# Performance work log

Hardware: AMD Instinct MI355X
Metric: run time of the kernel (lower is better)

The kernel has to match this reference:

```python
import jax, jax.numpy as jnp
import numpy as np

B, D, E, K = 8192, 4096, 64, 2

def setup_inputs() -> dict:
    key = jax.random.key(0)
    k1, k2 = jax.random.split(key)
    x = jax.random.normal(k1, (B, D), dtype=jnp.float32)
    gate_w = jax.random.normal(k2, (E, D), dtype=jnp.float32) * (1.0 / np.sqrt(D))
    temperature = jnp.ones((), dtype=jnp.float32)
    return {"x": x, "gate_w": gate_w, "temperature": temperature}

def reference(x, gate_w, temperature):
    # logits = (x @ W^T) / temperature  -> [B, E]
    logits = jnp.einsum('bd,ed->be', x, gate_w) / temperature
    top_logits, top_idx = jax.lax.top_k(logits, K)          # [B, K]
    routing_weights = jax.nn.softmax(top_logits, axis=-1)    # [B, K]
    rows = jnp.arange(x.shape[0])[:, None]                   # [B, 1]
    routing_matrix = jnp.zeros((x.shape[0], E), dtype=x.dtype).at[rows, top_idx].set(routing_weights)
    return routing_matrix, top_idx
```

## Files before the change

### kernel.cpp

```cpp
#include <hip/hip_runtime.h>
#include <stdint.h>
#include <stddef.h>


typedef __attribute__((ext_vector_type(8))) short short8;
typedef __attribute__((ext_vector_type(4))) float f32x4;

static constexpr int kB = 8192;
static constexpr int kD = 4096;
static constexpr int kE = 64;
static constexpr int kSteps = kD / 32;
static constexpr int kChunks = 16;
static constexpr int kStepsPerChunk = kSteps / kChunks;

__device__ __forceinline__ uint32_t bf16_rne(float v) {
    uint32_t u = __builtin_bit_cast(uint32_t, v);
    return (u + 0x7FFFu + ((u >> 16) & 1u)) >> 16;
}

__global__ __launch_bounds__(256) void prep_w_kernel(
    const float* __restrict__ w, short* __restrict__ w_hi, short* __restrict__ w_lo)
{
    int tid  = blockIdx.x * 256 + threadIdx.x;
    int lane = tid & 63;
    int s    = (tid >> 6) & (kSteps - 1);
    int nt   = tid >> 13;
    int e = nt * 16 + (lane & 15);
    int k = s * 32 + (lane >> 4) * 8;
    const float* src = w + (size_t)e * kD + k;
    short8 hi, lo;
#pragma unroll
    for (int j = 0; j < 8; ++j) {
        float xv = src[j];
        uint32_t u  = __builtin_bit_cast(uint32_t, xv);
        uint32_t rh = (u + 0x7FFFu + ((u >> 16) & 1u)) & 0xFFFF0000u;
        hi[j] = (short)(rh >> 16);
        float lf = xv - __builtin_bit_cast(float, rh);
        lo[j] = (short)bf16_rne(lf);
    }
    ((short8*)w_hi)[tid] = hi;
    ((short8*)w_lo)[tid] = lo;
}

__global__ __launch_bounds__(1024, 4) void router_kernel(
    const float* __restrict__ x, const short8* __restrict__ w_hi,
    const short8* __restrict__ w_lo, const float* __restrict__ temp,
    float* __restrict__ out_mat, float* __restrict__ out_idx)
{
    const int lane = threadIdx.x & 63;
    const int wv   = threadIdx.x >> 6;
    const int quad = lane >> 4;
    const int mr   = lane & 15;
    const int row0 = blockIdx.x * 16;

    const float* xp = x + (size_t)(row0 + mr) * kD
                        + wv * (kStepsPerChunk * 32) + quad * 8;

    f32x4 acc[4];
#pragma unroll
    for (int nt = 0; nt < 4; ++nt) acc[nt] = (f32x4){0.f, 0.f, 0.f, 0.f};

#pragma unroll 2
    for (int i = 0; i < kStepsPerChunk; ++i) {
        const f32x4* ap = (const f32x4*)(xp + i * 32);
        f32x4 a0 = ap[0];
        f32x4 a1 = ap[1];
        short8 ah, al;
#pragma unroll
        for (int j = 0; j < 4; ++j) {
            float xv = a0[j];
            uint32_t u  = __builtin_bit_cast(uint32_t, xv);
            uint32_t rh = (u + 0x7FFFu + ((u >> 16) & 1u)) & 0xFFFF0000u;
            ah[j] = (short)(rh >> 16);
            al[j] = (short)bf16_rne(xv - __builtin_bit_cast(float, rh));
            float yv = a1[j];
            uint32_t u2  = __builtin_bit_cast(uint32_t, yv);
            uint32_t rh2 = (u2 + 0x7FFFu + ((u2 >> 16) & 1u)) & 0xFFFF0000u;
            ah[j + 4] = (short)(rh2 >> 16);
            al[j + 4] = (short)bf16_rne(yv - __builtin_bit_cast(float, rh2));
        }
        const int sbase = (wv * kStepsPerChunk + i) * 64 + lane;
#pragma unroll
        for (int nt = 0; nt < 4; ++nt) {
            short8 wh_ = w_hi[(size_t)(nt * kSteps) * 64 + sbase];
            short8 wl_ = w_lo[(size_t)(nt * kSteps) * 64 + sbase];
            acc[nt] = __builtin_amdgcn_mfma_f32_16x16x32_bf16(al, wl_, acc[nt], 0, 0, 0);
            acc[nt] = __builtin_amdgcn_mfma_f32_16x16x32_bf16(al, wh_, acc[nt], 0, 0, 0);
            acc[nt] = __builtin_amdgcn_mfma_f32_16x16x32_bf16(ah, wl_, acc[nt], 0, 0, 0);
            acc[nt] = __builtin_amdgcn_mfma_f32_16x16x32_bf16(ah, wh_, acc[nt], 0, 0, 0);
        }
    }

    __shared__ float part[kChunks * 16 * kE];
#pragma unroll
    for (int nt = 0; nt < 4; ++nt)
#pragma unroll
        for (int r = 0; r < 4; ++r)
            part[(wv * 16 + quad * 4 + r) * kE + nt * 16 + mr] = acc[nt][r];
    __syncthreads();

    const int row = wv;
    float v = 0.f;
#pragma unroll
    for (int kc = 0; kc < kChunks; ++kc)
        v += part[(kc * 16 + row) * kE + lane];

    float v1 = v; int i1 = lane;
#pragma unroll
    for (int m = 1; m < 64; m <<= 1) {
        float ov = __shfl_xor(v1, m, 64);
        int   oi = __shfl_xor(i1, m, 64);
        if (ov > v1 || (ov == v1 && oi < i1)) { v1 = ov; i1 = oi; }
    }
    float vm = (lane == i1) ? -3.0e38f : v;
    float v2 = vm; int i2 = lane;
#pragma unroll
    for (int m = 1; m < 64; m <<= 1) {
        float ov = __shfl_xor(v2, m, 64);
        int   oi = __shfl_xor(i2, m, 64);
        if (ov > v2 || (ov == v2 && oi < i2)) { v2 = ov; i2 = oi; }
    }

    float invT = 1.0f / temp[0];
    float e  = expf((v2 - v1) * invT);
    float sm = 1.0f + e;
    float w1 = 1.0f / sm;
    float w2 = e / sm;

    out_mat[(size_t)(row0 + row) * kE + lane] = (lane == i1) ? w1
                                              : ((lane == i2) ? w2 : 0.0f);
    if (lane == 0) {
        ((float2*)out_idx)[row0 + row] = make_float2((float)i1, (float)i2);
    }
}

extern "C" void kernel_launch(void* const* d_in, const int* in_sizes, int n_in,
                              void* d_out, int out_size, void* d_ws, size_t ws_size,
                              hipStream_t stream) {
    const float* x    = (const float*)d_in[0];
    const float* gw   = (const float*)d_in[1];
    const float* temp = (const float*)d_in[2];

    float* out_mat = (float*)d_out;
    float* out_idx = (float*)d_out + (size_t)kB * kE;

    short* w_hi = (short*)d_ws;
    short* w_lo = w_hi + (size_t)kE * kD;

    prep_w_kernel<<<128, 256, 0, stream>>>(gw, w_hi, w_lo);

    router_kernel<<<kB / 16, 1024, 0, stream>>>(
        x, (const short8*)w_hi, (const short8*)w_lo, temp, out_mat, out_idx);
}
```

Baseline: 218.6 us.

## Halve waves per block and double-buffer x loads with register prefetch

The block shrinks from 16 to 8 waves, so each wave covers twice as many K steps. The x loads are now software-pipelined: the next pair of steps is prefetched into registers while the current pair is converted and fed to the MFMA units. The reduction step sums 8 partial sums instead of 16, and each wave finalises two rows. The aim is to hide global load latency and cut shared-memory and reduction overhead, at the cost of higher register pressure and fewer waves per block.

```diff
diff --git a/kernel.cpp b/kernel.cpp
--- a/kernel.cpp
+++ b/kernel.cpp
@@ -10,12 +10,30 @@
 static constexpr int kD = 4096;
 static constexpr int kE = 64;
 static constexpr int kSteps = kD / 32;
-static constexpr int kChunks = 16;
-static constexpr int kStepsPerChunk = kSteps / kChunks;
+static constexpr int kWv = 8;
+static constexpr int kSPC = kSteps / kWv;
+static constexpr int kRows = 16;
 
 __device__ __forceinline__ uint32_t bf16_rne(float v) {
     uint32_t u = __builtin_bit_cast(uint32_t, v);
     return (u + 0x7FFFu + ((u >> 16) & 1u)) >> 16;
+}
+
+__device__ __forceinline__ void cvt8(const f32x4& a0, const f32x4& a1,
+                                     short8& ah, short8& al) {
+#pragma unroll
+    for (int j = 0; j < 4; ++j) {
+        float xv = a0[j];
+        uint32_t u  = __builtin_bit_cast(uint32_t, xv);
+        uint32_t rh = (u + 0x7FFFu + ((u >> 16) & 1u)) & 0xFFFF0000u;
+        ah[j] = (short)(rh >> 16);
+        al[j] = (short)bf16_rne(xv - __builtin_bit_cast(float, rh));
+        float yv = a1[j];
+        uint32_t u2  = __builtin_bit_cast(uint32_t, yv);
+        uint32_t rh2 = (u2 + 0x7FFFu + ((u2 >> 16) & 1u)) & 0xFFFF0000u;
+        ah[j + 4] = (short)(rh2 >> 16);
+        al[j + 4] = (short)bf16_rne(yv - __builtin_bit_cast(float, rh2));
+    }
 }
 
 __global__ __launch_bounds__(256) void prep_w_kernel(
@@ -42,7 +60,7 @@
     ((short8*)w_lo)[tid] = lo;
 }
 
-__global__ __launch_bounds__(1024, 4) void router_kernel(
+__global__ __launch_bounds__(512, 4) void router_kernel(
     const float* __restrict__ x, const short8* __restrict__ w_hi,
     const short8* __restrict__ w_lo, const float* __restrict__ temp,
     float* __restrict__ out_mat, float* __restrict__ out_idx)
@@ -51,86 +69,88 @@
     const int wv   = threadIdx.x >> 6;
     const int quad = lane >> 4;
     const int mr   = lane & 15;
-    const int row0 = blockIdx.x * 16;
+    const int row0 = blockIdx.x * kRows;
 
-    const float* xp = x + (size_t)(row0 + mr) * kD
-                        + wv * (kStepsPerChunk * 32) + quad * 8;
+    const float* xp = x + (size_t)(row0 + mr) * kD + wv * (kSPC * 32) + quad * 8;
 
     f32x4 acc[4];
 #pragma unroll
     for (int nt = 0; nt < 4; ++nt) acc[nt] = (f32x4){0.f, 0.f, 0.f, 0.f};
 
-#pragma unroll 2
-    for (int i = 0; i < kStepsPerChunk; ++i) {
-        const f32x4* ap = (const f32x4*)(xp + i * 32);
-        f32x4 a0 = ap[0];
-        f32x4 a1 = ap[1];
-        short8 ah, al;
+    f32x4 xb[2][2][2];
 #pragma unroll
-        for (int j = 0; j < 4; ++j) {
-            float xv = a0[j];
-            uint32_t u  = __builtin_bit_cast(uint32_t, xv);
-            uint32_t rh = (u + 0x7FFFu + ((u >> 16) & 1u)) & 0xFFFF0000u;
-            ah[j] = (short)(rh >> 16);
-            al[j] = (short)bf16_rne(xv - __builtin_bit_cast(float, rh));
-            float yv = a1[j];
-            uint32_t u2  = __builtin_bit_cast(uint32_t, yv);
-            uint32_t rh2 = (u2 + 0x7FFFu + ((u2 >> 16) & 1u)) & 0xFFFF0000u;
-            ah[j + 4] = (short)(rh2 >> 16);
-            al[j + 4] = (short)bf16_rne(yv - __builtin_bit_cast(float, rh2));
+    for (int st = 0; st < 2; ++st) {
+        const f32x4* ap = (const f32x4*)(xp + st * 32);
+        xb[0][st][0] = ap[0];
+        xb[0][st][1] = ap[1];
+    }
+
+    for (int g = 0; g < kSPC / 2; ++g) {
+        const int cur = g & 1, nxt = cur ^ 1;
+        if (g + 1 < kSPC / 2) {
+#pragma unroll
+            for (int st = 0; st < 2; ++st) {
+                const f32x4* ap = (const f32x4*)(xp + ((g + 1) * 2 + st) * 32);
+                xb[nxt][st][0] = ap[0];
+                xb[nxt][st][1] = ap[1];
+            }
         }
-        const int sbase = (wv * kStepsPerChunk + i) * 64 + lane;
 #pragma unroll
-        for (int nt = 0; nt < 4; ++nt) {
-            short8 wh_ = w_hi[(size_t)(nt * kSteps) * 64 + sbase];
-            short8 wl_ = w_lo[(size_t)(nt * kSteps) * 64 + sbase];
-            acc[nt] = __builtin_amdgcn_mfma_f32_16x16x32_bf16(al, wl_, acc[nt], 0, 0, 0);
-            acc[nt] = __builtin_amdgcn_mfma_f32_16x16x32_bf16(al, wh_, acc[nt], 0, 0, 0);
-            acc[nt] = __builtin_amdgcn_mfma_f32_16x16x32_bf16(ah, wl_, acc[nt], 0, 0, 0);
-            acc[nt] = __builtin_amdgcn_mfma_f32_16x16x32_bf16(ah, wh_, acc[nt], 0, 0, 0);
+        for (int st = 0; st < 2; ++st) {
+            short8 ah, al;
+            cvt8(xb[cur][st][0], xb[cur][st][1], ah, al);
+            const size_t sb = (size_t)(wv * kSPC + g * 2 + st) * 64 + lane;
+#pragma unroll
+            for (int nt = 0; nt < 4; ++nt) {
+                short8 wh_ = w_hi[(size_t)(nt * kSteps) * 64 + sb];
+                short8 wl_ = w_lo[(size_t)(nt * kSteps) * 64 + sb];
+                acc[nt] = __builtin_amdgcn_mfma_f32_16x16x32_bf16(al, wl_, acc[nt], 0, 0, 0);
+                acc[nt] = __builtin_amdgcn_mfma_f32_16x16x32_bf16(al, wh_, acc[nt], 0, 0, 0);
+                acc[nt] = __builtin_amdgcn_mfma_f32_16x16x32_bf16(ah, wl_, acc[nt], 0, 0, 0);
+                acc[nt] = __builtin_amdgcn_mfma_f32_16x16x32_bf16(ah, wh_, acc[nt], 0, 0, 0);
+            }
         }
     }
 
-    __shared__ float part[kChunks * 16 * kE];
+    __shared__ float part[kWv][kRows][kE];
 #pragma unroll
     for (int nt = 0; nt < 4; ++nt)
 #pragma unroll
         for (int r = 0; r < 4; ++r)
-            part[(wv * 16 + quad * 4 + r) * kE + nt * 16 + mr] = acc[nt][r];
+            part[wv][quad * 4 + r][nt * 16 + mr] = acc[nt][r];
     __syncthreads();
 
-    const int row = wv;
-    float v = 0.f;
+    const float invT = 1.0f / temp[0];
 #pragma unroll
-    for (int kc = 0; kc < kChunks; ++kc)
-        v += part[(kc * 16 + row) * kE + lane];
+    for (int p = 0; p < 2; ++p) {
+        const int row = wv + p * kWv;
+        float v = 0.f;
+#pragma unroll
+        for (int s = 0; s < kWv; ++s)
+            v += part[s][row][lane];
 
-    float v1 = v; int i1 = lane;
+        float v1 = v; int i1 = lane;
 #pragma unroll
-    for (int m = 1; m < 64; m <<= 1) {
-        float ov = __shfl_xor(v1, m, 64);
-        int   oi = __shfl_xor(i1, m, 64);
-        if (ov > v1 || (ov == v1 && oi < i1)) { v1 = ov; i1 = oi; }
-    }
-    float vm = (lane == i1) ? -3.0e38f : v;
-    float v2 = vm; int i2 = lane;
+        for (int m = 1; m < 64; m <<= 1) {
+            float ov = __shfl_xor(v1, m, 64);
+            int   oi = __shfl_xor(i1, m, 64);
+            if (ov > v1 || (ov == v1 && oi < i1)) { v1 = ov; i1 = oi; }
+        }
+        float vm = (lane == i1) ? -3.0e38f : v;
+        float v2 = vm; int i2 = lane;
 #pragma unroll
-    for (int m = 1; m < 64; m <<= 1) {
-        float ov = __shfl_xor(v2, m, 64);
-        int   oi = __shfl_xor(i2, m, 64);
-        if (ov > v2 || (ov == v2 && oi < i2)) { v2 = ov; i2 = oi; }
-    }
+        for (int m = 1; m < 64; m <<= 1) {
+            float ov = __shfl_xor(v2, m, 64);
+            int   oi = __shfl_xor(i2, m, 64);
+            if (ov > v2 || (ov == v2 && oi < i2)) { v2 = ov; i2 = oi; }
+        }
 
-    float invT = 1.0f / temp[0];
-    float e  = expf((v2 - v1) * invT);
-    float sm = 1.0f + e;
-    float w1 = 1.0f / sm;
-    float w2 = e / sm;
-
-    out_mat[(size_t)(row0 + row) * kE + lane] = (lane == i1) ? w1
-                                              : ((lane == i2) ? w2 : 0.0f);
-    if (lane == 0) {
-        ((float2*)out_idx)[row0 + row] = make_float2((float)i1, (float)i2);
+        float e  = expf((v2 - v1) * invT);
+        float sm = 1.0f + e;
+        out_mat[(size_t)(row0 + row) * kE + lane] =
+            (lane == i1) ? (1.0f / sm) : ((lane == i2) ? (e / sm) : 0.0f);
+        if (lane == 0)
+            ((float2*)out_idx)[row0 + row] = make_float2((float)i1, (float)i2);
     }
 }
 
@@ -149,6 +169,6 @@
 
     prep_w_kernel<<<128, 256, 0, stream>>>(gw, w_hi, w_lo);
 
-    router_kernel<<<kB / 16, 1024, 0, stream>>>(
+    router_kernel<<<kB / kRows, 512, 0, stream>>>(
         x, (const short8*)w_hi, (const short8*)w_lo, temp, out_mat, out_idx);
 }
```

Measured after the change: 213.5 us. 1.02x faster.
